# Kernel tuning notes

Hardware: AMD Instinct MI355X
Metric: run time of the kernel (lower is better)

## Reference

```python
import jax, jax.numpy as jnp
import numpy as np

N_NODES = 50000
N_EDGES = 1600000
HEADS = 4
HIDE = 32
OUT = 32
IN_CH = 128
NEG_SLOPE = 0.2


def setup_inputs() -> dict:
    key = jax.random.key(0)
    ks = jax.random.split(key, 12)
    return {
        "x": jax.random.normal(ks[0], (N_NODES, IN_CH), dtype=jnp.float32),
        "edge_index": jax.random.randint(ks[1], (2, N_EDGES), 0, N_NODES, dtype=jnp.int64),
        "root_index": jax.random.randint(ks[2], (64,), 0, N_NODES, dtype=jnp.int64),
        "W1": jax.random.normal(ks[3], (IN_CH, HEADS * HIDE), dtype=jnp.float32) * 0.1,
        "a1_src": jax.random.normal(ks[4], (HEADS, HIDE), dtype=jnp.float32) * 0.1,
        "a1_dst": jax.random.normal(ks[5], (HEADS, HIDE), dtype=jnp.float32) * 0.1,
        "b1": jnp.zeros((HEADS * HIDE,), dtype=jnp.float32),
        "W2": jax.random.normal(ks[6], (HEADS * HIDE, HEADS * OUT), dtype=jnp.float32) * 0.1,
        "a2_src": jax.random.normal(ks[7], (HEADS, OUT), dtype=jnp.float32) * 0.1,
        "a2_dst": jax.random.normal(ks[8], (HEADS, OUT), dtype=jnp.float32) * 0.1,
        "b2": jnp.zeros((HEADS * OUT,), dtype=jnp.float32),
    }


def gat_conv(x, W, a_src, a_dst, b, src, dst, n_nodes, heads, d_out):
    # per-head linear transform: [N, heads, d_out]
    h = (x @ W).reshape(n_nodes, heads, d_out)
    # per-node attention logit halves: [N, heads]
    alpha_s = jnp.einsum("nhd,hd->nh", h, a_src)
    alpha_d = jnp.einsum("nhd,hd->nh", h, a_dst)
    # per-edge unnormalized logits: [E, heads]
    e = jax.nn.leaky_relu(alpha_s[src] + alpha_d[dst], negative_slope=NEG_SLOPE)
    # segment softmax over incoming edges of each destination node
    e_max = jax.ops.segment_max(e, dst, num_segments=n_nodes)
    e_exp = jnp.exp(e - e_max[dst])
    denom = jax.ops.segment_sum(e_exp, dst, num_segments=n_nodes)
    alpha = e_exp / (denom[dst] + 1e-16)
    # weighted scatter-aggregate of source features
    msg = h[src] * alpha[:, :, None]  # [E, heads, d_out]
    out = jax.ops.segment_sum(msg, dst, num_segments=n_nodes)
    return out.reshape(n_nodes, heads * d_out) + b


def reference(x, edge_index, root_index, W1, a1_src, a1_dst, b1, W2, a2_src, a2_dst, b2):
    n = x.shape[0]
    loops = jnp.arange(n, dtype=edge_index.dtype)
    src = jnp.concatenate([edge_index[0], loops])
    dst = jnp.concatenate([edge_index[1], loops])
    h = gat_conv(x, W1, a1_src, a1_dst, b1, src, dst, n, HEADS, HIDE)
    h = jax.nn.relu(h)
    out = gat_conv(h, W2, a2_src, a2_dst, b2, src, dst, n, HEADS, OUT)
    return out[root_index].reshape(-1, out.shape[-1])
```

## Files before the change

### kernel.cpp

```cpp
#include <hip/hip_runtime.h>
#include <hip/hip_bf16.h>

#define N_NODES 50000
#define N_EDGES 1600000
#define NVEC4 (N_EDGES / 4)
#define HEADS 4
#define NEG_SLOPE 0.2f
#define CAP 16384
#define CAPDEG 256
#define NCOL 144
#define WT_L (NCOL * 128)
#define NBW 784
#define TSTRIDE 148

typedef short short8 __attribute__((ext_vector_type(8)));
typedef float f32x4 __attribute__((ext_vector_type(4)));

__device__ __forceinline__ float leaky(float x) { return fmaxf(x, NEG_SLOPE * x); }

__device__ __forceinline__ unsigned short f2bf(float f) {
    unsigned int u = __builtin_bit_cast(unsigned int, f);
    u += 0x7fffu + ((u >> 16) & 1u);
    return (unsigned short)(u >> 16);
}
__device__ __forceinline__ float bf2f(unsigned short s) {
    unsigned int u = ((unsigned int)s) << 16;
    return __builtin_bit_cast(float, u);
}

__device__ __forceinline__ int sidx(int col, int k) {
    return ((col * 128 + (k & ~7)) ^ ((col & 7) << 3)) + (k & 7);
}


__global__ __launch_bounds__(256) void k1_kernel(const float* __restrict__ W1,
                            const float* __restrict__ a1s, const float* __restrict__ a1d,
                            const float* __restrict__ W2,
                            const float* __restrict__ a2s, const float* __restrict__ a2d,
                            const int* __restrict__ ei, const int* __restrict__ rts,
                            unsigned short* __restrict__ wt_hi, unsigned short* __restrict__ wt_lo,
                            int* __restrict__ flag1, int* __restrict__ mdeg,
                            int* __restrict__ cnt) {
    __shared__ unsigned long long lmask[NBW];
    int t = threadIdx.x;
    int tid = blockIdx.x * 256 + t;
    for (int w = t; w < NBW; w += 256) lmask[w] = 0ull;
    __syncthreads();
    if (t < 64) {
        int n = rts[t];
        atomicOr(&lmask[n >> 6], 1ull << (n & 63));
        if (blockIdx.x == 0) flag1[n] = 1;
    }
    __syncthreads();

    if (tid < CAP) mdeg[tid] = 0;
    if (tid == 0) *cnt = 0;

    if (tid < 2 * WT_L) {
        int layer = tid / WT_L;
        int rem = tid - layer * WT_L;
        int col = rem >> 7;
        int k = rem & 127;
        const float* W = layer ? W2 : W1;
        const float* as = layer ? a2s : a1s;
        const float* ad = layer ? a2d : a1d;
        float w = 0.f;
        if (col < 128) {
            w = W[k * 128 + col];
        } else if (col < 136) {
            int j = col - 128;
            int h = j & 3;
            const float* av = (j < 4) ? as : ad;
            float s = 0.f;
            for (int d = 0; d < 32; ++d) s += W[k * 128 + h * 32 + d] * av[h * 32 + d];
            w = s;
        }
        unsigned short hb = f2bf(w);
        int si = layer * WT_L + sidx(col, k);
        wt_hi[si] = hb;
        wt_lo[si] = f2bf(w - bf2f(hb));
    }

    if (tid < NVEC4) {
        int4 s4 = ((const int4*)ei)[tid];
        int4 d4 = ((const int4*)(ei + N_EDGES))[tid];
        int ss[4] = {s4.x, s4.y, s4.z, s4.w};
        int dd[4] = {d4.x, d4.y, d4.z, d4.w};
#pragma unroll
        for (int j = 0; j < 4; ++j)
            if ((lmask[dd[j] >> 6] >> (dd[j] & 63)) & 1ull) flag1[ss[j]] = 1;
    }
}


__global__ __launch_bounds__(256) void compact_kernel(const int* __restrict__ flag1,
                                                      int* __restrict__ cnt,
                                                      int* __restrict__ list,
                                                      int* __restrict__ inv,
                                                      unsigned long long* __restrict__ f1bits) {
    int i = blockIdx.x * blockDim.x + threadIdx.x;
    int lane = threadIdx.x & 63;
    int f = (i < N_NODES) ? (flag1[i] == 1) : 0;
    unsigned long long b = __ballot(f != 0);
    if (lane == 0) f1bits[i >> 6] = b;
    if (b) {
        int leader = (int)(__ffsll((long long)b) - 1);
        int base = 0;
        if (lane == leader) base = atomicAdd(cnt, __popcll(b));
        base = __shfl(base, leader, 64);
        if (f) {
            int p = base + __popcll(b & ((1ull << lane) - 1ull));
            if (p < CAP) { list[p] = i; inv[i] = p; }
        }
    }
}


template <int RELU, int DYN>
__device__ __forceinline__ void gemm_body(const float* __restrict__ A,
                                          const unsigned short* __restrict__ wt_hi,
                                          const unsigned short* __restrict__ wt_lo,
                                          float* __restrict__ H,
                                          float* __restrict__ aS, float* __restrict__ aD,
                                          int n_static, const int* __restrict__ cntp,
                                          int tile0, int tstep, float* smem) {
    short* shw = (short*)smem;
    int n = DYN ? *cntp : n_static;
    if (DYN && n > CAP) n = CAP;
    int ntiles = (n + 127) >> 7;
    int t = threadIdx.x;
    int w = t >> 6;
    int l = t & 63;
    int lr = l & 15;
    int lq = l >> 4;
    for (int tile = tile0; tile < ntiles; tile += tstep) {
        for (int s = t; s < 2 * NCOL * 16; s += 512) {
            int half = s >= NCOL * 16;
            int rem = half ? s - NCOL * 16 : s;
            const unsigned short* src = half ? wt_lo : wt_hi;
            short8 v = *(const short8*)(src + rem * 8);
            *(short8*)(shw + half * WT_L + rem * 8) = v;
        }
        __syncthreads();
        int row0 = tile * 128;
        int wrow = row0 + w * 16;
        f32x4 acc[9];
#pragma unroll
        for (int ct = 0; ct < 9; ++ct) acc[ct] = (f32x4){0.f, 0.f, 0.f, 0.f};
#pragma unroll
        for (int kk = 0; kk < 4; ++kk) {
            int gr = wrow + lr;
            float4 p0 = make_float4(0.f, 0.f, 0.f, 0.f);
            float4 p1 = make_float4(0.f, 0.f, 0.f, 0.f);
            if (gr < n) {
                const float* p = A + (size_t)gr * 128 + kk * 32 + lq * 8;
                p0 = *(const float4*)p;
                p1 = *(const float4*)(p + 4);
            }
            short8 ah, al;
            float xv[8] = {p0.x, p0.y, p0.z, p0.w, p1.x, p1.y, p1.z, p1.w};
#pragma unroll
            for (int j = 0; j < 8; ++j) {
                float f = RELU ? fmaxf(xv[j], 0.f) : xv[j];
                unsigned short hb = f2bf(f);
                ah[j] = (short)hb;
                al[j] = (short)f2bf(f - bf2f(hb));
            }
#pragma unroll
            for (int ct = 0; ct < 9; ++ct) {
                int col = ct * 16 + lr;
                int base = (col * 128 + kk * 32 + lq * 8) ^ ((col & 7) << 3);
                short8 bh = *(const short8*)(shw + base);
                short8 bl = *(const short8*)(shw + base + WT_L);
                acc[ct] = __builtin_amdgcn_mfma_f32_16x16x32_bf16(ah, bh, acc[ct], 0, 0, 0);
                acc[ct] = __builtin_amdgcn_mfma_f32_16x16x32_bf16(ah, bl, acc[ct], 0, 0, 0);
                acc[ct] = __builtin_amdgcn_mfma_f32_16x16x32_bf16(al, bh, acc[ct], 0, 0, 0);
                acc[ct] = __builtin_amdgcn_mfma_f32_16x16x32_bf16(al, bl, acc[ct], 0, 0, 0);
            }
        }
        __syncthreads();
#pragma unroll
        for (int ct = 0; ct < 9; ++ct) {
#pragma unroll
            for (int r = 0; r < 4; ++r)
                smem[(w * 16 + lq * 4 + r) * TSTRIDE + ct * 16 + lr] = acc[ct][r];
        }
        __syncthreads();
#pragma unroll
        for (int i = 0; i < 8; ++i) {
            int idx = t + i * 512;
            int row = idx >> 5;
            int c4 = idx & 31;
            int gr = row0 + row;
            if (gr < n)
                *(float4*)(H + (size_t)gr * 128 + c4 * 4) = *(const float4*)&smem[row * TSTRIDE + c4 * 4];
        }
        if (t < 256) {
            int row = t >> 1, q = t & 1;
            int gr = row0 + row;
            if (gr < n) {
                float4 v = *(const float4*)&smem[row * TSTRIDE + 128 + q * 4];
                if (q == 0) *(float4*)(aS + (size_t)gr * 4) = v;
                else        *(float4*)(aD + (size_t)gr * 4) = v;
            }
        }
        __syncthreads();
    }
}


__global__ __launch_bounds__(512) void k34_kernel(const float* __restrict__ x,
                                                  const unsigned short* __restrict__ wt_hi,
                                                  const unsigned short* __restrict__ wt_lo,
                                                  float* __restrict__ H,
                                                  float* __restrict__ aS, float* __restrict__ aD,
                                                  const int* __restrict__ ei,
                                                  const unsigned long long* __restrict__ f1bits,
                                                  const int* __restrict__ inv,
                                                  int* __restrict__ mdeg, int* __restrict__ bucket) {
    __shared__ float smem[128 * TSTRIDE];
    int b = blockIdx.x;
    int t = threadIdx.x;
    if (b < 391) {
        gemm_body<0, 0>(x, wt_hi, wt_lo, H, aS, aD, N_NODES, nullptr, b, 455, smem);
    } else {
        unsigned long long* lmask = (unsigned long long*)smem;
        for (int wd = t; wd < NBW; wd += 512) lmask[wd] = f1bits[wd];
        __syncthreads();
        for (int i = (b - 391) * 512 + t; i < NVEC4; i += 64 * 512) {
            int4 s4 = ((const int4*)ei)[i];
            int4 d4 = ((const int4*)(ei + N_EDGES))[i];
            int ss[4] = {s4.x, s4.y, s4.z, s4.w};
            int dd[4] = {d4.x, d4.y, d4.z, d4.w};
#pragma unroll
            for (int j = 0; j < 4; ++j) {
                if ((lmask[dd[j] >> 6] >> (dd[j] & 63)) & 1ull) {
                    unsigned row = (unsigned)inv[dd[j]];
                    if (row < CAP) {
                        int sl = atomicAdd(&mdeg[row], 1);
                        if (sl < CAPDEG) bucket[row * CAPDEG + sl] = ss[j];
                    }
                }
            }
        }
    }
}


__global__ __launch_bounds__(512) void gemm2_kernel(const float* __restrict__ A,
                                                    const unsigned short* __restrict__ wt_hi,
                                                    const unsigned short* __restrict__ wt_lo,
                                                    float* __restrict__ H,
                                                    float* __restrict__ aS, float* __restrict__ aD,
                                                    const int* __restrict__ cntp) {
    __shared__ float smem[128 * TSTRIDE];
    gemm_body<1, 1>(A, wt_hi, wt_lo, H, aS, aD, 0, cntp, blockIdx.x, gridDim.x, smem);
}


template <int MODE>
__global__ __launch_bounds__(512) void agg_kernel(const float* __restrict__ H,
                                                  const float* __restrict__ aS,
                                                  const float* __restrict__ aD,
                                                  const int* __restrict__ mdeg,
                                                  const int* __restrict__ bucket,
                                                  const float* __restrict__ bias,
                                                  const int* __restrict__ list,
                                                  const int* __restrict__ inv,
                                                  const int* __restrict__ cntp,
                                                  float* __restrict__ out) {
    __shared__ float asmem[8 * 1284];
    int t = threadIdx.x;
    int wb = t >> 6;
    int lane = t & 63;
    int h = lane >> 4;
    int* s_src = (int*)&asmem[wb * 1284];
    float* s_w = &asmem[wb * 1284 + 256];
    int cnt = MODE ? 64 : *cntp;
    if (cnt > CAP) cnt = CAP;
    float2 bv = ((const float2*)bias)[lane];
    int wv = blockIdx.x * 8 + wb;
    int nw = gridDim.x * 8;
    for (int j = wv; j < cnt; j += nw) {
        int n = list[j];
        int row = MODE ? inv[n] : j;
        int own = MODE ? row : n;
        int deg = mdeg[row]; if (deg > CAPDEG) deg = CAPDEG;
        float4 adv = ((const float4*)aD)[own];
        for (int i = lane; i < deg; i += 64) {
            int s = bucket[row * CAPDEG + i];
            int si = MODE ? inv[s] : s;
            s_src[i] = si;
            float4 a4 = ((const float4*)aS)[si];
            s_w[0 * 257 + i] = __expf(leaky(a4.x + adv.x));
            s_w[1 * 257 + i] = __expf(leaky(a4.y + adv.y));
            s_w[2 * 257 + i] = __expf(leaky(a4.z + adv.z));
            s_w[3 * 257 + i] = __expf(leaky(a4.w + adv.w));
        }
        float ash = aS[own * 4 + h];
        float adh = aD[own * 4 + h];
        float w_self = __expf(leaky(ash + adh));
        asm volatile("s_waitcnt lgkmcnt(0)" ::: "memory");
        float denom = w_self;
        const float2* Hr = (const float2*)(H + (size_t)own * 128);
        float2 hv0 = Hr[lane];
        float2 acc = make_float2(w_self * hv0.x, w_self * hv0.y);
        for (int i = 0; i < deg; ++i) {
            float wgt = s_w[h * 257 + i];
            float2 hv = ((const float2*)(H + (size_t)s_src[i] * 128))[lane];
            denom += wgt;
            acc.x += wgt * hv.x;
            acc.y += wgt * hv.y;
        }
        float2 o = make_float2(acc.x / denom + bv.x, acc.y / denom + bv.y);
        ((float2*)out)[(size_t)j * 64 + lane] = o;
    }
}


extern "C" void kernel_launch(void* const* d_in, const int* in_sizes, int n_in,
                              void* d_out, int out_size, void* d_ws, size_t ws_size,
                              hipStream_t stream) {
    const float* x   = (const float*)d_in[0];
    const int*   ei  = (const int*)d_in[1];
    const int*   rts = (const int*)d_in[2];
    const float* W1  = (const float*)d_in[3];
    const float* a1s = (const float*)d_in[4];
    const float* a1d = (const float*)d_in[5];
    const float* b1  = (const float*)d_in[6];
    const float* W2  = (const float*)d_in[7];
    const float* a2s = (const float*)d_in[8];
    const float* a2d = (const float*)d_in[9];
    const float* b2  = (const float*)d_in[10];
    float* out = (float*)d_out;

    char* ws = (char*)d_ws;
    size_t o = 0;
    auto alloc = [&](size_t bytes) -> void* {
        void* p = ws + o;
        o += (bytes + 255) & ~(size_t)255;
        return p;
    };
    int* flag1 = (int*)alloc((size_t)N_NODES * 4);
    int* cnt   = (int*)alloc(4);
    int* mdeg  = (int*)alloc((size_t)CAP * 4);
    unsigned long long* f1bits = (unsigned long long*)alloc((size_t)NBW * 8);
    int* list  = (int*)alloc((size_t)CAP * 4);
    int* inv   = (int*)alloc((size_t)N_NODES * 4);
    int* bucket = (int*)alloc((size_t)CAP * CAPDEG * 4);
    unsigned short* wt_hi = (unsigned short*)alloc((size_t)2 * WT_L * 2);
    unsigned short* wt_lo = (unsigned short*)alloc((size_t)2 * WT_L * 2);
    float* h1  = (float*)alloc((size_t)N_NODES * 128 * 4);
    float* aS1 = (float*)alloc((size_t)N_NODES * HEADS * 4);
    float* aD1 = (float*)alloc((size_t)N_NODES * HEADS * 4);
    float* o1c = (float*)alloc((size_t)CAP * 128 * 4);
    float* h2c = (float*)alloc((size_t)CAP * 128 * 4);
    float* aS2 = (float*)alloc((size_t)CAP * HEADS * 4);
    float* aD2 = (float*)alloc((size_t)CAP * HEADS * 4);

    k1_kernel<<<(NVEC4 + 255) / 256, 256, 0, stream>>>(W1, a1s, a1d, W2, a2s, a2d,
                                                       ei, rts, wt_hi, wt_lo, flag1, mdeg, cnt);
    compact_kernel<<<(NBW * 64) / 256, 256, 0, stream>>>(flag1, cnt, list, inv, f1bits);
    k34_kernel<<<455, 512, 0, stream>>>(x, wt_hi, wt_lo, h1, aS1, aD1,
                                        ei, f1bits, inv, mdeg, bucket);
    agg_kernel<0><<<256, 512, 0, stream>>>(h1, aS1, aD1, mdeg, bucket, b1, list, inv, cnt, o1c);
    gemm2_kernel<<<32, 512, 0, stream>>>(o1c, wt_hi + WT_L, wt_lo + WT_L, h2c, aS2, aD2, cnt);
    agg_kernel<1><<<8, 512, 0, stream>>>(h2c, aS2, aD2, mdeg, bucket, b2, rts, inv, cnt, out);
}
```

Baseline: 183.0 us.

## Split fused gemm/edge-pass kernel; read weights from global instead of LDS

Breaks the combined k34 kernel into a standalone edge-bucketing kernel and a separate GEMM kernel. The GEMM now uses 64-row tiles with 256 threads, one tile per block and an occupancy hint. It reads B fragments straight from global/L2 in an unswizzled layout instead of staging the weight matrix into shared memory. This removes the per-tile LDS weight copy and its barriers, and lets more blocks run concurrently. In exchange, the edge pass and the first GEMM are serialized on the stream instead of overlapping, and weight loads go through cache rather than LDS.

```diff
diff --git a/kernel.cpp b/kernel.cpp
--- a/kernel.cpp
+++ b/kernel.cpp
@@ -26,10 +26,6 @@
 __device__ __forceinline__ float bf2f(unsigned short s) {
     unsigned int u = ((unsigned int)s) << 16;
     return __builtin_bit_cast(float, u);
-}
-
-__device__ __forceinline__ int sidx(int col, int k) {
-    return ((col * 128 + (k & ~7)) ^ ((col & 7) << 3)) + (k & 7);
 }
 
 
@@ -76,7 +72,7 @@
             w = s;
         }
         unsigned short hb = f2bf(w);
-        int si = layer * WT_L + sidx(col, k);
+        int si = layer * WT_L + col * 128 + k;
         wt_hi[si] = hb;
         wt_lo[si] = f2bf(w - bf2f(hb));
     }
@@ -116,145 +112,114 @@
 }
 
 
+__global__ __launch_bounds__(256) void passE_kernel(const int* __restrict__ ei,
+                                                    const unsigned long long* __restrict__ f1bits,
+                                                    const int* __restrict__ inv,
+                                                    int* __restrict__ mdeg,
+                                                    int* __restrict__ bucket) {
+    __shared__ unsigned long long lmask[NBW];
+    int t = threadIdx.x;
+    for (int w = t; w < NBW; w += 256) lmask[w] = f1bits[w];
+    __syncthreads();
+    int i = blockIdx.x * 256 + t;
+    if (i >= NVEC4) return;
+    int4 s4 = ((const int4*)ei)[i];
+    int4 d4 = ((const int4*)(ei + N_EDGES))[i];
+    int ss[4] = {s4.x, s4.y, s4.z, s4.w};
+    int dd[4] = {d4.x, d4.y, d4.z, d4.w};
+#pragma unroll
+    for (int j = 0; j < 4; ++j) {
+        if ((lmask[dd[j] >> 6] >> (dd[j] & 63)) & 1ull) {
+            unsigned row = (unsigned)inv[dd[j]];
+            if (row < CAP) {
+                int sl = atomicAdd(&mdeg[row], 1);
+                if (sl < CAPDEG) bucket[row * CAPDEG + sl] = ss[j];
+            }
+        }
+    }
+}
+
+
 template <int RELU, int DYN>
-__device__ __forceinline__ void gemm_body(const float* __restrict__ A,
-                                          const unsigned short* __restrict__ wt_hi,
-                                          const unsigned short* __restrict__ wt_lo,
-                                          float* __restrict__ H,
-                                          float* __restrict__ aS, float* __restrict__ aD,
-                                          int n_static, const int* __restrict__ cntp,
-                                          int tile0, int tstep, float* smem) {
-    short* shw = (short*)smem;
+__global__ __launch_bounds__(256, 3) void gemm_kernel(const float* __restrict__ A,
+                                                      const unsigned short* __restrict__ wt_hi,
+                                                      const unsigned short* __restrict__ wt_lo,
+                                                      float* __restrict__ H,
+                                                      float* __restrict__ aS,
+                                                      float* __restrict__ aD,
+                                                      int n_static, const int* __restrict__ cntp) {
+    __shared__ float smem[64 * TSTRIDE];
     int n = DYN ? *cntp : n_static;
     if (DYN && n > CAP) n = CAP;
-    int ntiles = (n + 127) >> 7;
+    int ntiles = (n + 63) >> 6;
+    int tile = blockIdx.x;
+    if (tile >= ntiles) return;
     int t = threadIdx.x;
     int w = t >> 6;
     int l = t & 63;
     int lr = l & 15;
     int lq = l >> 4;
-    for (int tile = tile0; tile < ntiles; tile += tstep) {
-        for (int s = t; s < 2 * NCOL * 16; s += 512) {
-            int half = s >= NCOL * 16;
-            int rem = half ? s - NCOL * 16 : s;
-            const unsigned short* src = half ? wt_lo : wt_hi;
-            short8 v = *(const short8*)(src + rem * 8);
-            *(short8*)(shw + half * WT_L + rem * 8) = v;
-        }
-        __syncthreads();
-        int row0 = tile * 128;
-        int wrow = row0 + w * 16;
-        f32x4 acc[9];
-#pragma unroll
-        for (int ct = 0; ct < 9; ++ct) acc[ct] = (f32x4){0.f, 0.f, 0.f, 0.f};
-#pragma unroll
-        for (int kk = 0; kk < 4; ++kk) {
-            int gr = wrow + lr;
-            float4 p0 = make_float4(0.f, 0.f, 0.f, 0.f);
-            float4 p1 = make_float4(0.f, 0.f, 0.f, 0.f);
-            if (gr < n) {
-                const float* p = A + (size_t)gr * 128 + kk * 32 + lq * 8;
-                p0 = *(const float4*)p;
-                p1 = *(const float4*)(p + 4);
-            }
-            short8 ah, al;
-            float xv[8] = {p0.x, p0.y, p0.z, p0.w, p1.x, p1.y, p1.z, p1.w};
-#pragma unroll
-            for (int j = 0; j < 8; ++j) {
-                float f = RELU ? fmaxf(xv[j], 0.f) : xv[j];
-                unsigned short hb = f2bf(f);
-                ah[j] = (short)hb;
-                al[j] = (short)f2bf(f - bf2f(hb));
-            }
-#pragma unroll
-            for (int ct = 0; ct < 9; ++ct) {
-                int col = ct * 16 + lr;
-                int base = (col * 128 + kk * 32 + lq * 8) ^ ((col & 7) << 3);
-                short8 bh = *(const short8*)(shw + base);
-                short8 bl = *(const short8*)(shw + base + WT_L);
-                acc[ct] = __builtin_amdgcn_mfma_f32_16x16x32_bf16(ah, bh, acc[ct], 0, 0, 0);
-                acc[ct] = __builtin_amdgcn_mfma_f32_16x16x32_bf16(ah, bl, acc[ct], 0, 0, 0);
-                acc[ct] = __builtin_amdgcn_mfma_f32_16x16x32_bf16(al, bh, acc[ct], 0, 0, 0);
-                acc[ct] = __builtin_amdgcn_mfma_f32_16x16x32_bf16(al, bl, acc[ct], 0, 0, 0);
-            }
-        }
-        __syncthreads();
+    int row0 = tile * 64;
+    int wrow = row0 + w * 16;
+    f32x4 acc[9];
+#pragma unroll
+    for (int ct = 0; ct < 9; ++ct) acc[ct] = (f32x4){0.f, 0.f, 0.f, 0.f};
+#pragma unroll
+    for (int kk = 0; kk < 4; ++kk) {
+        int gr = wrow + lr;
+        float4 p0 = make_float4(0.f, 0.f, 0.f, 0.f);
+        float4 p1 = make_float4(0.f, 0.f, 0.f, 0.f);
+        if (gr < n) {
+            const float* p = A + (size_t)gr * 128 + kk * 32 + lq * 8;
+            p0 = *(const float4*)p;
+            p1 = *(const float4*)(p + 4);
+        }
+        short8 ah, al;
+        float xv[8] = {p0.x, p0.y, p0.z, p0.w, p1.x, p1.y, p1.z, p1.w};
+#pragma unroll
+        for (int j = 0; j < 8; ++j) {
+            float f = RELU ? fmaxf(xv[j], 0.f) : xv[j];
+            unsigned short hb = f2bf(f);
+            ah[j] = (short)hb;
+            al[j] = (short)f2bf(f - bf2f(hb));
+        }
+        const unsigned short* bhp = wt_hi + lr * 128 + kk * 32 + lq * 8;
+        const unsigned short* blp = wt_lo + lr * 128 + kk * 32 + lq * 8;
 #pragma unroll
         for (int ct = 0; ct < 9; ++ct) {
-#pragma unroll
-            for (int r = 0; r < 4; ++r)
-                smem[(w * 16 + lq * 4 + r) * TSTRIDE + ct * 16 + lr] = acc[ct][r];
-        }
-        __syncthreads();
-#pragma unroll
-        for (int i = 0; i < 8; ++i) {
-            int idx = t + i * 512;
-            int row = idx >> 5;
-            int c4 = idx & 31;
-            int gr = row0 + row;
-            if (gr < n)
-                *(float4*)(H + (size_t)gr * 128 + c4 * 4) = *(const float4*)&smem[row * TSTRIDE + c4 * 4];
-        }
-        if (t < 256) {
-            int row = t >> 1, q = t & 1;
-            int gr = row0 + row;
-            if (gr < n) {
-                float4 v = *(const float4*)&smem[row * TSTRIDE + 128 + q * 4];
-                if (q == 0) *(float4*)(aS + (size_t)gr * 4) = v;
-                else        *(float4*)(aD + (size_t)gr * 4) = v;
-            }
-        }
-        __syncthreads();
-    }
-}
-
-
-__global__ __launch_bounds__(512) void k34_kernel(const float* __restrict__ x,
-                                                  const unsigned short* __restrict__ wt_hi,
-                                                  const unsigned short* __restrict__ wt_lo,
-                                                  float* __restrict__ H,
-                                                  float* __restrict__ aS, float* __restrict__ aD,
-                                                  const int* __restrict__ ei,
-                                                  const unsigned long long* __restrict__ f1bits,
-                                                  const int* __restrict__ inv,
-                                                  int* __restrict__ mdeg, int* __restrict__ bucket) {
-    __shared__ float smem[128 * TSTRIDE];
-    int b = blockIdx.x;
-    int t = threadIdx.x;
-    if (b < 391) {
-        gemm_body<0, 0>(x, wt_hi, wt_lo, H, aS, aD, N_NODES, nullptr, b, 455, smem);
-    } else {
-        unsigned long long* lmask = (unsigned long long*)smem;
-        for (int wd = t; wd < NBW; wd += 512) lmask[wd] = f1bits[wd];
-        __syncthreads();
-        for (int i = (b - 391) * 512 + t; i < NVEC4; i += 64 * 512) {
-            int4 s4 = ((const int4*)ei)[i];
-            int4 d4 = ((const int4*)(ei + N_EDGES))[i];
-            int ss[4] = {s4.x, s4.y, s4.z, s4.w};
-            int dd[4] = {d4.x, d4.y, d4.z, d4.w};
-#pragma unroll
-            for (int j = 0; j < 4; ++j) {
-                if ((lmask[dd[j] >> 6] >> (dd[j] & 63)) & 1ull) {
-                    unsigned row = (unsigned)inv[dd[j]];
-                    if (row < CAP) {
-                        int sl = atomicAdd(&mdeg[row], 1);
-                        if (sl < CAPDEG) bucket[row * CAPDEG + sl] = ss[j];
-                    }
-                }
-            }
-        }
-    }
-}
-
-
-__global__ __launch_bounds__(512) void gemm2_kernel(const float* __restrict__ A,
-                                                    const unsigned short* __restrict__ wt_hi,
-                                                    const unsigned short* __restrict__ wt_lo,
-                                                    float* __restrict__ H,
-                                                    float* __restrict__ aS, float* __restrict__ aD,
-                                                    const int* __restrict__ cntp) {
-    __shared__ float smem[128 * TSTRIDE];
-    gemm_body<1, 1>(A, wt_hi, wt_lo, H, aS, aD, 0, cntp, blockIdx.x, gridDim.x, smem);
+            short8 bh = *(const short8*)(bhp + ct * 2048);
+            short8 bl = *(const short8*)(blp + ct * 2048);
+            acc[ct] = __builtin_amdgcn_mfma_f32_16x16x32_bf16(ah, bh, acc[ct], 0, 0, 0);
+            acc[ct] = __builtin_amdgcn_mfma_f32_16x16x32_bf16(ah, bl, acc[ct], 0, 0, 0);
+            acc[ct] = __builtin_amdgcn_mfma_f32_16x16x32_bf16(al, bh, acc[ct], 0, 0, 0);
+            acc[ct] = __builtin_amdgcn_mfma_f32_16x16x32_bf16(al, bl, acc[ct], 0, 0, 0);
+        }
+    }
+#pragma unroll
+    for (int ct = 0; ct < 9; ++ct) {
+#pragma unroll
+        for (int r = 0; r < 4; ++r)
+            smem[(w * 16 + lq * 4 + r) * TSTRIDE + ct * 16 + lr] = acc[ct][r];
+    }
+    __syncthreads();
+#pragma unroll
+    for (int i = 0; i < 8; ++i) {
+        int idx = t + i * 256;
+        int row = idx >> 5;
+        int c4 = idx & 31;
+        int gr = row0 + row;
+        if (gr < n)
+            *(float4*)(H + (size_t)gr * 128 + c4 * 4) = *(const float4*)&smem[row * TSTRIDE + c4 * 4];
+    }
+    if (t < 128) {
+        int row = t >> 1, q = t & 1;
+        int gr = row0 + row;
+        if (gr < n) {
+            float4 v = *(const float4*)&smem[row * TSTRIDE + 128 + q * 4];
+            if (q == 0) *(float4*)(aS + (size_t)gr * 4) = v;
+            else        *(float4*)(aD + (size_t)gr * 4) = v;
+        }
+    }
 }
 
 
@@ -361,9 +326,11 @@
     k1_kernel<<<(NVEC4 + 255) / 256, 256, 0, stream>>>(W1, a1s, a1d, W2, a2s, a2d,
                                                        ei, rts, wt_hi, wt_lo, flag1, mdeg, cnt);
     compact_kernel<<<(NBW * 64) / 256, 256, 0, stream>>>(flag1, cnt, list, inv, f1bits);
-    k34_kernel<<<455, 512, 0, stream>>>(x, wt_hi, wt_lo, h1, aS1, aD1,
-                                        ei, f1bits, inv, mdeg, bucket);
+    passE_kernel<<<(NVEC4 + 255) / 256, 256, 0, stream>>>(ei, f1bits, inv, mdeg, bucket);
+    gemm_kernel<0, 0><<<(N_NODES + 63) / 64, 256, 0, stream>>>(
+        x, wt_hi, wt_lo, h1, aS1, aD1, N_NODES, nullptr);
     agg_kernel<0><<<256, 512, 0, stream>>>(h1, aS1, aD1, mdeg, bucket, b1, list, inv, cnt, o1c);
-    gemm2_kernel<<<32, 512, 0, stream>>>(o1c, wt_hi + WT_L, wt_lo + WT_L, h2c, aS2, aD2, cnt);
+    gemm_kernel<1, 1><<<CAP / 64, 256, 0, stream>>>(
+        o1c, wt_hi + WT_L, wt_lo + WT_L, h2c, aS2, aD2, 0, cnt);
     agg_kernel<1><<<8, 512, 0, stream>>>(h2c, aS2, aD2, mdeg, bucket, b2, rts, inv, cnt, out);
 }
```

Result: slower. 187.9 us (+2.7%).
